# Performance work log

Hardware: AMD Instinct MI355X
Metric: run time of the kernel (lower is better)

## Reference

```python
import jax, jax.numpy as jnp
import numpy as np

D = 1024
H = 16
DH = D // H


def setup_inputs() -> dict:
    key = jax.random.key(0)
    ks = jax.random.split(key, 9)
    s = 1.0 / np.sqrt(D)
    return {
        "x": jax.random.normal(ks[0], (4, 2048, D), dtype=jnp.float32),
        "wq": jax.random.uniform(ks[1], (D, D), jnp.float32, -s, s),
        "bq": jax.random.uniform(ks[2], (D,), jnp.float32, -s, s),
        "wk": jax.random.uniform(ks[3], (D, D), jnp.float32, -s, s),
        "bk": jax.random.uniform(ks[4], (D,), jnp.float32, -s, s),
        "wv": jax.random.uniform(ks[5], (D, D), jnp.float32, -s, s),
        "bv": jax.random.uniform(ks[6], (D,), jnp.float32, -s, s),
        "wo": jax.random.uniform(ks[7], (D, D), jnp.float32, -s, s),
        "bo": jax.random.uniform(ks[8], (D,), jnp.float32, -s, s),
    }


def reference(x, wq, bq, wk, bk, wv, bv, wo, bo):
    B, S, _ = x.shape
    # projections + split heads: [B, S, D] -> [B, H, S, Dh]
    def split(t):
        return t.reshape(B, S, H, DH).transpose(0, 2, 1, 3)
    q = split(x @ wq + bq)
    k = split(x @ wk + bk)
    v = split(x @ wv + bv)
    scale = 1.0 / jnp.sqrt(jnp.float32(DH))
    scores = jnp.einsum("bhqd,bhkd->bhqk", q, k) * scale  # [B,H,S,S]
    att = jax.nn.softmax(scores, axis=-1)
    out = jnp.einsum("bhqk,bhkd->bhqd", att, v)  # [B,H,S,Dh]
    out = out.transpose(0, 2, 1, 3).reshape(B, S, D)
    return out @ wo + bo
```

## Files before the change

### kernel.cpp

```cpp
#include <hip/hip_runtime.h>
#include <stdint.h>

typedef float f32x4 __attribute__((ext_vector_type(4)));
typedef __bf16 bf16x8 __attribute__((ext_vector_type(8)));
typedef unsigned short ushort_t;
typedef ushort_t ushortx8 __attribute__((ext_vector_type(8)));
typedef ushort_t ushortx4 __attribute__((ext_vector_type(4)));

#define DEV static __device__ __forceinline__

DEV ushort_t f2bf(float f) {
  union { float f; uint32_t u; } v; v.f = f;
  uint32_t u = v.u;
  return (ushort_t)((u + 0x7FFFu + ((u >> 16) & 1u)) >> 16);
}

DEV uint32_t pkbf(float a, float b) {
  __bf16 x = (__bf16)a, y = (__bf16)b;
  return (uint32_t)__builtin_bit_cast(unsigned short, x) |
         ((uint32_t)__builtin_bit_cast(unsigned short, y) << 16);
}

DEV void cp16(const void* g, void* l) {
  __builtin_amdgcn_global_load_lds((const __attribute__((address_space(1))) unsigned int*)g,
                                   (__attribute__((address_space(3))) unsigned int*)l,
                                   16, 0, 0);
}

DEV f32x4 mfma16(bf16x8 a, bf16x8 b, f32x4 c) {
  return __builtin_amdgcn_mfma_f32_16x16x32_bf16(a, b, c, 0, 0, 0);
}

__global__ __launch_bounds__(256) void k_prep(
    const float* __restrict__ x, ushort_t* __restrict__ xb,
    const float* __restrict__ wq, const float* __restrict__ wk,
    const float* __restrict__ wv, const float* __restrict__ wo,
    ushort_t* __restrict__ wqkvT, ushort_t* __restrict__ woT) {
  __shared__ float tile[32][33];
  int b = blockIdx.x;
  if (b < 4096) {
    size_t idx = ((size_t)b * 256 + threadIdx.x) * 8;
    const float4* src = (const float4*)(x + idx);
    float4 a = src[0], c = src[1];
    ushortx8 o;
    o[0] = f2bf(a.x); o[1] = f2bf(a.y); o[2] = f2bf(a.z); o[3] = f2bf(a.w);
    o[4] = f2bf(c.x); o[5] = f2bf(c.y); o[6] = f2bf(c.z); o[7] = f2bf(c.w);
    *(ushortx8*)(xb + idx) = o;
  } else {
    int t = b - 4096;
    int which = t >> 10;
    const float* src = (which == 0) ? wq : (which == 1) ? wk : (which == 2) ? wv : wo;
    ushort_t* dst = (which == 0) ? wqkvT
                    : (which == 1) ? wqkvT + 1024 * 1024
                    : (which == 2) ? wqkvT + 2 * 1024 * 1024
                                   : woT;
    int tt = t & 1023;
    int c0 = (tt & 31) * 32, r0 = (tt >> 5) * 32;
    int tx = threadIdx.x & 31, ty = threadIdx.x >> 5;
#pragma unroll
    for (int i = ty; i < 32; i += 8)
      tile[i][tx] = src[(size_t)(r0 + i) * 1024 + c0 + tx];
    __syncthreads();
#pragma unroll
    for (int i = ty; i < 32; i += 8)
      dst[(size_t)(c0 + i) * 1024 + r0 + tx] = f2bf(tile[tx][i]);
  }
}

template <int MODE>
__global__ __launch_bounds__(512, 1) void k_gemm2(
    const ushort_t* __restrict__ A, const ushort_t* __restrict__ Bt,
    const float* __restrict__ b0, const float* __restrict__ b1,
    const float* __restrict__ b2, ushort_t* __restrict__ qw,
    ushort_t* __restrict__ kw, ushort_t* __restrict__ vtw,
    float* __restrict__ outf) {
  extern __shared__ ushort_t lds[];
  ushort_t* As3 = lds;
  ushort_t* Bs3 = lds + 3 * 8192;
  const int K = 1024, NT = 16;
  int tid = threadIdx.x;
  int w = tid >> 6, lane = tid & 63, l16 = lane & 15, lg = lane >> 4;
  int wr = w >> 2, wc = w & 3;
  int m0 = blockIdx.x * 128, n0 = blockIdx.y * 256;

  const ushort_t* Asrc = A + (size_t)(m0 + (tid >> 3)) * K +
                         (size_t)(((tid & 7) ^ ((tid >> 3) & 7)) * 8);
  const ushort_t* Bsrc = Bt + (size_t)(n0 + (tid >> 3)) * K +
                         (size_t)(((tid & 7) ^ ((tid >> 3) & 7)) * 8);

  f32x4 acc[4][4] = {};
  bf16x8 a[2][2], b[4][2];
  const int aRow = wr * 64 + l16, bRow = wc * 64 + l16, rsw = l16 & 7;

#pragma unroll
  for (int tt = 0; tt < 2; ++tt) {
    cp16(Asrc + (size_t)tt * 64, As3 + tt * 8192 + w * 512);
    cp16(Asrc + (size_t)tt * 64 + (size_t)64 * K, As3 + tt * 8192 + 4096 + w * 512);
#pragma unroll
    for (int s = 0; s < 4; ++s)
      cp16(Bsrc + (size_t)tt * 64 + (size_t)s * 64 * K,
           Bs3 + tt * 16384 + s * 4096 + w * 512);
  }
  asm volatile("s_waitcnt vmcnt(6)" ::: "memory");
  __builtin_amdgcn_s_barrier();

  int cur = 0, nx2 = 2;
  for (int t = 0; t < NT; ++t) {
    ushort_t* AsC = As3 + cur * 8192;
    ushort_t* BsC = Bs3 + cur * 16384;
    ushort_t* AsN = As3 + nx2 * 8192;
    ushort_t* BsN = Bs3 + nx2 * 16384;
    int t2 = (t + 2 < NT) ? t + 2 : NT - 1;
    const ushort_t* A2 = Asrc + (size_t)t2 * 64;
    const ushort_t* B2 = Bsrc + (size_t)t2 * 64;

#pragma unroll
    for (int i2 = 0; i2 < 2; ++i2)
#pragma unroll
      for (int ks = 0; ks < 2; ++ks)
        a[i2][ks] = *(const bf16x8*)&AsC[(aRow + i2 * 16) * 64 +
                                         (((ks << 2) | lg) ^ rsw) * 8];
#pragma unroll
    for (int j2 = 0; j2 < 2; ++j2)
#pragma unroll
      for (int ks = 0; ks < 2; ++ks)
        b[j2][ks] = *(const bf16x8*)&BsC[(bRow + j2 * 16) * 64 +
                                         (((ks << 2) | lg) ^ rsw) * 8];
    cp16(A2, AsN + w * 512);
    cp16(A2 + (size_t)64 * K, AsN + 4096 + w * 512);
    __builtin_amdgcn_s_barrier();
    asm volatile("s_waitcnt lgkmcnt(0)" ::: "memory");
    __builtin_amdgcn_s_setprio(1);
#pragma unroll
    for (int i2 = 0; i2 < 2; ++i2)
#pragma unroll
      for (int j2 = 0; j2 < 2; ++j2)
#pragma unroll
        for (int ks = 0; ks < 2; ++ks)
          acc[i2][j2] = mfma16(a[i2][ks], b[j2][ks], acc[i2][j2]);
    __builtin_amdgcn_s_setprio(0);
    __builtin_amdgcn_s_barrier();

#pragma unroll
    for (int j2 = 2; j2 < 4; ++j2)
#pragma unroll
      for (int ks = 0; ks < 2; ++ks)
        b[j2][ks] = *(const bf16x8*)&BsC[(bRow + j2 * 16) * 64 +
                                         (((ks << 2) | lg) ^ rsw) * 8];
    cp16(B2, BsN + w * 512);
    cp16(B2 + (size_t)64 * K, BsN + 4096 + w * 512);
    __builtin_amdgcn_s_barrier();
    asm volatile("s_waitcnt lgkmcnt(0)" ::: "memory");
    __builtin_amdgcn_s_setprio(1);
#pragma unroll
    for (int i2 = 0; i2 < 2; ++i2)
#pragma unroll
      for (int j2 = 2; j2 < 4; ++j2)
#pragma unroll
        for (int ks = 0; ks < 2; ++ks)
          acc[i2][j2] = mfma16(a[i2][ks], b[j2][ks], acc[i2][j2]);
    __builtin_amdgcn_s_setprio(0);
    __builtin_amdgcn_s_barrier();

#pragma unroll
    for (int i2 = 0; i2 < 2; ++i2)
#pragma unroll
      for (int ks = 0; ks < 2; ++ks)
        a[i2][ks] = *(const bf16x8*)&AsC[(aRow + (2 + i2) * 16) * 64 +
                                         (((ks << 2) | lg) ^ rsw) * 8];
    cp16(B2 + (size_t)2 * 64 * K, BsN + 8192 + w * 512);
    cp16(B2 + (size_t)3 * 64 * K, BsN + 12288 + w * 512);
    __builtin_amdgcn_s_barrier();
    asm volatile("s_waitcnt lgkmcnt(0)" ::: "memory");
    __builtin_amdgcn_s_setprio(1);
#pragma unroll
    for (int i2 = 0; i2 < 2; ++i2)
#pragma unroll
      for (int j2 = 2; j2 < 4; ++j2)
#pragma unroll
        for (int ks = 0; ks < 2; ++ks)
          acc[2 + i2][j2] = mfma16(a[i2][ks], b[j2][ks], acc[2 + i2][j2]);
    __builtin_amdgcn_s_setprio(0);
    __builtin_amdgcn_s_barrier();

    asm volatile("s_waitcnt vmcnt(6)" ::: "memory");
    __builtin_amdgcn_s_barrier();
    __builtin_amdgcn_s_setprio(1);
#pragma unroll
    for (int i2 = 0; i2 < 2; ++i2)
#pragma unroll
      for (int j2 = 0; j2 < 2; ++j2)
#pragma unroll
        for (int ks = 0; ks < 2; ++ks)
          acc[2 + i2][j2] = mfma16(a[i2][ks], b[j2][ks], acc[2 + i2][j2]);
    __builtin_amdgcn_s_setprio(0);
    __builtin_amdgcn_s_barrier();

    cur = (cur + 1 == 3) ? 0 : cur + 1;
    nx2 = (nx2 + 1 == 3) ? 0 : nx2 + 1;
  }

  if (MODE == 0) {
    const float QSCALE = 0.18033688011112042f;
    int p = blockIdx.x >> 3;
    int cbase = (m0 & 1023) + wr * 64;
    if (p == 2) {
#pragma unroll
      for (int i = 0; i < 4; ++i) {
        int oc = cbase + i * 16 + lg * 4;
        int h = oc >> 6, dh0 = oc & 63;
        float4 bb = *(const float4*)&b2[oc];
#pragma unroll
        for (int j = 0; j < 4; ++j) {
          int tok = n0 + wc * 64 + j * 16 + l16;
          int bi = tok >> 11, tk = tok & 2047;
          size_t vb = ((size_t)((bi * 16 + h) * 64 + dh0)) * 2048 + tk;
          vtw[vb] = f2bf(acc[i][j][0] + bb.x);
          vtw[vb + 2048] = f2bf(acc[i][j][1] + bb.y);
          vtw[vb + 2 * 2048] = f2bf(acc[i][j][2] + bb.z);
          vtw[vb + 3 * 2048] = f2bf(acc[i][j][3] + bb.w);
        }
      }
    } else {
      const float* bias = (p == 0) ? b0 : b1;
      ushort_t* dst = (p == 0) ? qw : kw;
      float qs = (p == 0) ? QSCALE : 1.0f;
#pragma unroll
      for (int i = 0; i < 4; ++i) {
        int oc = cbase + i * 16 + lg * 4;
        int h = oc >> 6, dh0 = oc & 63;
        float4 bb = *(const float4*)&bias[oc];
#pragma unroll
        for (int j = 0; j < 4; ++j) {
          int tok = n0 + wc * 64 + j * 16 + l16;
          size_t base =
              ((size_t)((tok >> 11) * 16 + h) * 2048 + (tok & 2047)) * 64 + dh0;
          ushortx4 pk;
          pk[0] = f2bf((acc[i][j][0] + bb.x) * qs);
          pk[1] = f2bf((acc[i][j][1] + bb.y) * qs);
          pk[2] = f2bf((acc[i][j][2] + bb.z) * qs);
          pk[3] = f2bf((acc[i][j][3] + bb.w) * qs);
          *(ushortx4*)&dst[base] = pk;
        }
      }
    }
  } else {
#pragma unroll
    for (int j = 0; j < 4; ++j) {
      int col = n0 + wc * 64 + j * 16 + l16;
      float bb = b0[col];
#pragma unroll
      for (int i = 0; i < 4; ++i) {
#pragma unroll
        for (int r = 0; r < 4; ++r) {
          int row = m0 + wr * 64 + i * 16 + lg * 4 + r;
          outf[(size_t)row * 1024 + col] = acc[i][j][r] + bb;
        }
      }
    }
  }
}

__global__ __launch_bounds__(512, 2) void k_attn(
    const ushort_t* __restrict__ qg, const ushort_t* __restrict__ kg,
    const ushort_t* __restrict__ vtg, ushort_t* __restrict__ att) {
  __shared__ ushort_t Ks[2][64 * 64];
  __shared__ ushort_t Vs[2][64 * 64];
  __shared__ ushort_t Ps[8][16 * 128];
  int tid = threadIdx.x;
  int w = tid >> 6, lane = tid & 63, l16 = lane & 15, lg = lane >> 4;
  int i = blockIdx.x;
  int bh = (i & 7) * 8 + ((i >> 3) & 7);
  int q0 = (i >> 6) * 256;
  const ushort_t* qh = qg + (size_t)bh * 2048 * 64;

  const ushort_t* kstage = kg + (size_t)bh * 2048 * 64 + (size_t)(tid >> 3) * 64 +
                           (size_t)(((tid & 7) ^ ((tid >> 3) & 7)) * 8);
  const ushort_t* vstage = vtg + (size_t)bh * 64 * 2048 + (size_t)(tid >> 3) * 2048 +
                           (size_t)(((tid & 7) ^ ((tid >> 3) & 7)) * 8);

  bf16x8 qf[2][2];
#pragma unroll
  for (int st = 0; st < 2; ++st)
#pragma unroll
    for (int ks = 0; ks < 2; ++ks)
      qf[st][ks] = *(const bf16x8*)(qh + (size_t)(q0 + w * 32 + st * 16 + l16) * 64 +
                                    ks * 32 + lg * 8);

  bf16x8 vone;
#pragma unroll
  for (int t = 0; t < 8; ++t) vone[t] = (__bf16)1.0f;

  f32x4 o[2][5] = {};

  cp16(kstage, &Ks[0][tid * 8]);
  cp16(vstage, &Vs[0][tid * 8]);
  __syncthreads();

  for (int t = 0; t < 32; ++t) {
    int cur = t & 1, nxt = cur ^ 1;
    cp16(kstage + (size_t)(t + 1) * 64 * 64, &Ks[nxt][tid * 8]);
    cp16(vstage + (size_t)(t + 1) * 64, &Vs[nxt][tid * 8]);

    f32x4 sc[2][4] = {};
    __builtin_amdgcn_s_setprio(1);
#pragma unroll
    for (int jt = 0; jt < 4; ++jt) {
      int row = jt * 16 + l16;
      bf16x8 kf0 = *(const bf16x8*)&Ks[cur][row * 64 + ((lg) ^ (l16 & 7)) * 8];
      bf16x8 kf1 = *(const bf16x8*)&Ks[cur][row * 64 + ((lg + 4) ^ (l16 & 7)) * 8];
      sc[0][jt] = mfma16(kf0, qf[0][0], sc[0][jt]);
      sc[0][jt] = mfma16(kf1, qf[0][1], sc[0][jt]);
      sc[1][jt] = mfma16(kf0, qf[1][0], sc[1][jt]);
      sc[1][jt] = mfma16(kf1, qf[1][1], sc[1][jt]);
    }
    __builtin_amdgcn_s_setprio(0);

#pragma unroll
    for (int st = 0; st < 2; ++st)
#pragma unroll
      for (int jt = 0; jt < 4; ++jt) {
        float e0 = __builtin_amdgcn_exp2f(sc[st][jt][0]);
        float e1 = __builtin_amdgcn_exp2f(sc[st][jt][1]);
        float e2 = __builtin_amdgcn_exp2f(sc[st][jt][2]);
        float e3 = __builtin_amdgcn_exp2f(sc[st][jt][3]);
        uint2 pk2;
        pk2.x = pkbf(e0, e1);
        pk2.y = pkbf(e2, e3);
        *(uint2*)&Ps[w][l16 * 128 +
                        (((st * 8 + jt * 2 + (lg >> 1)) ^ l16) * 8) +
                        (lg & 1) * 4] = pk2;
      }

    __builtin_amdgcn_s_setprio(1);
#pragma unroll
    for (int ks = 0; ks < 2; ++ks) {
      bf16x8 pf0 =
          *(const bf16x8*)&Ps[w][l16 * 128 + (((ks * 4 + lg) ^ l16) * 8)];
      bf16x8 pf1 =
          *(const bf16x8*)&Ps[w][l16 * 128 + (((8 + ks * 4 + lg) ^ l16) * 8)];
      o[0][4] = mfma16(pf0, vone, o[0][4]);
      o[1][4] = mfma16(pf1, vone, o[1][4]);
#pragma unroll
      for (int dt = 0; dt < 4; ++dt) {
        int vrow = dt * 16 + l16;
        bf16x8 vf =
            *(const bf16x8*)&Vs[cur][vrow * 64 + (((ks * 4 + lg) ^ (l16 & 7)) * 8)];
        o[0][dt] = mfma16(pf0, vf, o[0][dt]);
        o[1][dt] = mfma16(pf1, vf, o[1][dt]);
      }
    }
    __builtin_amdgcn_s_setprio(0);

    __syncthreads();
  }

  int bi = bh >> 4, h = bh & 15;
#pragma unroll
  for (int st = 0; st < 2; ++st) {
    f32x4 inv;
#pragma unroll
    for (int r = 0; r < 4; ++r) inv[r] = __builtin_amdgcn_rcpf(o[st][4][r]);
#pragma unroll
    for (int dt = 0; dt < 4; ++dt)
#pragma unroll
      for (int r = 0; r < 4; ++r) {
        int srow = q0 + w * 32 + st * 16 + lg * 4 + r;
        int col = h * 64 + dt * 16 + l16;
        att[(size_t)(bi * 2048 + srow) * 1024 + col] = f2bf(o[st][dt][r] * inv[r]);
      }
  }
}

extern "C" void kernel_launch(void* const* d_in, const int* in_sizes, int n_in,
                              void* d_out, int out_size, void* d_ws, size_t ws_size,
                              hipStream_t stream) {
  const float* x = (const float*)d_in[0];
  const float* wq = (const float*)d_in[1];
  const float* bq = (const float*)d_in[2];
  const float* wk = (const float*)d_in[3];
  const float* bk = (const float*)d_in[4];
  const float* wv = (const float*)d_in[5];
  const float* bv = (const float*)d_in[6];
  const float* wo = (const float*)d_in[7];
  const float* bo = (const float*)d_in[8];
  float* out = (float*)d_out;

  char* ws = (char*)d_ws;
  ushort_t* xb = (ushort_t*)(ws);
  ushort_t* wqkvT = (ushort_t*)(ws + 16777216);
  ushort_t* woT = (ushort_t*)(ws + 23068672);
  ushort_t* qw = (ushort_t*)(ws + 25165824);
  ushort_t* kw = (ushort_t*)(ws + 41943040);
  ushort_t* vtw = (ushort_t*)(ws + 58720256);
  ushort_t* att = (ushort_t*)(ws + 75497472);

  k_prep<<<dim3(8192), dim3(256), 0, stream>>>(x, xb, wq, wk, wv, wo, wqkvT, woT);

  const int G2_LDS = 147456;
  hipFuncSetAttribute(reinterpret_cast<const void*>(&k_gemm2<0>),
                      hipFuncAttributeMaxDynamicSharedMemorySize, G2_LDS);
  hipFuncSetAttribute(reinterpret_cast<const void*>(&k_gemm2<1>),
                      hipFuncAttributeMaxDynamicSharedMemorySize, G2_LDS);

  k_gemm2<0><<<dim3(24, 32), dim3(512), G2_LDS, stream>>>(
      wqkvT, xb, bq, bk, bv, qw, kw, vtw, nullptr);

  k_attn<<<dim3(512), dim3(512), 0, stream>>>(qw, kw, vtw, att);

  k_gemm2<1><<<dim3(64, 4), dim3(512), G2_LDS, stream>>>(
      att, woT, bo, nullptr, nullptr, nullptr, nullptr, nullptr, out);
}
```

Baseline: 259.1 us.

## Fuse prep, QKV GEMM, attention and output GEMM into one cooperative persistent kernel

Replaces four separate kernel launches with a single cooperative kernel of 256 persistent blocks that run each stage in turn, separated by grid-wide syncs. Each block loops over the QKV GEMM tiles (3 per block) and the attention units (2 per block), and does one output GEMM tile. The GEMM's clamped tail prefetches now write into a dead LDS region, and a full drain is added at the end of each tile so LDS can be reused safely. The aim is to remove launch gaps and tail effects between kernels. In exchange, attention now runs at one block per CU instead of two, and the grid syncs add cost.

```diff
diff --git a/kernel.cpp b/kernel.cpp
--- a/kernel.cpp
+++ b/kernel.cpp
@@ -1,5 +1,8 @@
 #include <hip/hip_runtime.h>
+#include <hip/hip_cooperative_groups.h>
 #include <stdint.h>
+
+namespace cg = cooperative_groups;
 
 typedef float f32x4 __attribute__((ext_vector_type(4)));
 typedef __bf16 bf16x8 __attribute__((ext_vector_type(8)));
@@ -31,57 +34,59 @@
   return __builtin_amdgcn_mfma_f32_16x16x32_bf16(a, b, c, 0, 0, 0);
 }
 
-__global__ __launch_bounds__(256) void k_prep(
-    const float* __restrict__ x, ushort_t* __restrict__ xb,
-    const float* __restrict__ wq, const float* __restrict__ wk,
-    const float* __restrict__ wv, const float* __restrict__ wo,
-    ushort_t* __restrict__ wqkvT, ushort_t* __restrict__ woT) {
-  __shared__ float tile[32][33];
-  int b = blockIdx.x;
-  if (b < 4096) {
-    size_t idx = ((size_t)b * 256 + threadIdx.x) * 8;
+#define DEAD_OFF 73728
+
+DEV void prep_phase(int bid, int tid, const float* x, ushort_t* xb,
+                    const float* wq, const float* wk, const float* wv,
+                    const float* wo, ushort_t* wqkvT, ushort_t* woT,
+                    ushort_t* lds) {
+  int gtid = bid * 512 + tid;
+  for (int c = gtid; c < 1048576; c += 131072) {
+    size_t idx = (size_t)c * 8;
     const float4* src = (const float4*)(x + idx);
-    float4 a = src[0], c = src[1];
+    float4 a = src[0], cc = src[1];
     ushortx8 o;
     o[0] = f2bf(a.x); o[1] = f2bf(a.y); o[2] = f2bf(a.z); o[3] = f2bf(a.w);
-    o[4] = f2bf(c.x); o[5] = f2bf(c.y); o[6] = f2bf(c.z); o[7] = f2bf(c.w);
+    o[4] = f2bf(cc.x); o[5] = f2bf(cc.y); o[6] = f2bf(cc.z); o[7] = f2bf(cc.w);
     *(ushortx8*)(xb + idx) = o;
-  } else {
-    int t = b - 4096;
-    int which = t >> 10;
+  }
+  float* tf = (float*)lds;
+  int sub = tid >> 8, stid = tid & 255;
+  int tx = stid & 31, ty = stid >> 5;
+  float* tile = tf + sub * 1056;
+  for (int it = 0; it < 8; ++it) {
+    int v = bid * 16 + it * 2 + sub;
+    int which = v >> 10;
     const float* src = (which == 0) ? wq : (which == 1) ? wk : (which == 2) ? wv : wo;
     ushort_t* dst = (which == 0) ? wqkvT
                     : (which == 1) ? wqkvT + 1024 * 1024
                     : (which == 2) ? wqkvT + 2 * 1024 * 1024
                                    : woT;
-    int tt = t & 1023;
+    int tt = v & 1023;
     int c0 = (tt & 31) * 32, r0 = (tt >> 5) * 32;
-    int tx = threadIdx.x & 31, ty = threadIdx.x >> 5;
+    __syncthreads();
 #pragma unroll
     for (int i = ty; i < 32; i += 8)
-      tile[i][tx] = src[(size_t)(r0 + i) * 1024 + c0 + tx];
+      tile[i * 33 + tx] = src[(size_t)(r0 + i) * 1024 + c0 + tx];
     __syncthreads();
 #pragma unroll
     for (int i = ty; i < 32; i += 8)
-      dst[(size_t)(c0 + i) * 1024 + r0 + tx] = f2bf(tile[tx][i]);
+      dst[(size_t)(c0 + i) * 1024 + r0 + tx] = f2bf(tile[tx * 33 + i]);
   }
 }
 
 template <int MODE>
-__global__ __launch_bounds__(512, 1) void k_gemm2(
-    const ushort_t* __restrict__ A, const ushort_t* __restrict__ Bt,
-    const float* __restrict__ b0, const float* __restrict__ b1,
-    const float* __restrict__ b2, ushort_t* __restrict__ qw,
-    ushort_t* __restrict__ kw, ushort_t* __restrict__ vtw,
-    float* __restrict__ outf) {
-  extern __shared__ ushort_t lds[];
+DEV void gemm_tile(const ushort_t* A, const ushort_t* Bt, const float* b0,
+                   const float* b1, const float* b2, ushort_t* qw,
+                   ushort_t* kw, ushort_t* vtw, float* outf, int bx, int by,
+                   int tid, ushort_t* lds) {
   ushort_t* As3 = lds;
   ushort_t* Bs3 = lds + 3 * 8192;
+  ushort_t* dead = lds + DEAD_OFF;
   const int K = 1024, NT = 16;
-  int tid = threadIdx.x;
   int w = tid >> 6, lane = tid & 63, l16 = lane & 15, lg = lane >> 4;
   int wr = w >> 2, wc = w & 3;
-  int m0 = blockIdx.x * 128, n0 = blockIdx.y * 256;
+  int m0 = bx * 128, n0 = by * 256;
 
   const ushort_t* Asrc = A + (size_t)(m0 + (tid >> 3)) * K +
                          (size_t)(((tid & 7) ^ ((tid >> 3) & 7)) * 8);
@@ -108,9 +113,14 @@
   for (int t = 0; t < NT; ++t) {
     ushort_t* AsC = As3 + cur * 8192;
     ushort_t* BsC = Bs3 + cur * 16384;
-    ushort_t* AsN = As3 + nx2 * 8192;
-    ushort_t* BsN = Bs3 + nx2 * 16384;
-    int t2 = (t + 2 < NT) ? t + 2 : NT - 1;
+    bool live = (t + 2 < NT);
+    ushort_t* AsN = live ? As3 + nx2 * 8192 : dead;
+    ushort_t* BsN = live ? Bs3 + nx2 * 16384 : dead;
+    int a4096 = live ? 4096 : 0;
+    int b4096 = live ? 4096 : 0;
+    int b8192 = live ? 8192 : 0;
+    int b12288 = live ? 12288 : 0;
+    int t2 = live ? t + 2 : NT - 1;
     const ushort_t* A2 = Asrc + (size_t)t2 * 64;
     const ushort_t* B2 = Bsrc + (size_t)t2 * 64;
 
@@ -127,7 +137,7 @@
         b[j2][ks] = *(const bf16x8*)&BsC[(bRow + j2 * 16) * 64 +
                                          (((ks << 2) | lg) ^ rsw) * 8];
     cp16(A2, AsN + w * 512);
-    cp16(A2 + (size_t)64 * K, AsN + 4096 + w * 512);
+    cp16(A2 + (size_t)64 * K, AsN + a4096 + w * 512);
     __builtin_amdgcn_s_barrier();
     asm volatile("s_waitcnt lgkmcnt(0)" ::: "memory");
     __builtin_amdgcn_s_setprio(1);
@@ -148,7 +158,7 @@
         b[j2][ks] = *(const bf16x8*)&BsC[(bRow + j2 * 16) * 64 +
                                          (((ks << 2) | lg) ^ rsw) * 8];
     cp16(B2, BsN + w * 512);
-    cp16(B2 + (size_t)64 * K, BsN + 4096 + w * 512);
+    cp16(B2 + (size_t)64 * K, BsN + b4096 + w * 512);
     __builtin_amdgcn_s_barrier();
     asm volatile("s_waitcnt lgkmcnt(0)" ::: "memory");
     __builtin_amdgcn_s_setprio(1);
@@ -168,8 +178,8 @@
       for (int ks = 0; ks < 2; ++ks)
         a[i2][ks] = *(const bf16x8*)&AsC[(aRow + (2 + i2) * 16) * 64 +
                                          (((ks << 2) | lg) ^ rsw) * 8];
-    cp16(B2 + (size_t)2 * 64 * K, BsN + 8192 + w * 512);
-    cp16(B2 + (size_t)3 * 64 * K, BsN + 12288 + w * 512);
+    cp16(B2 + (size_t)2 * 64 * K, BsN + b8192 + w * 512);
+    cp16(B2 + (size_t)3 * 64 * K, BsN + b12288 + w * 512);
     __builtin_amdgcn_s_barrier();
     asm volatile("s_waitcnt lgkmcnt(0)" ::: "memory");
     __builtin_amdgcn_s_setprio(1);
@@ -199,10 +209,12 @@
     cur = (cur + 1 == 3) ? 0 : cur + 1;
     nx2 = (nx2 + 1 == 3) ? 0 : nx2 + 1;
   }
+  asm volatile("s_waitcnt vmcnt(0)" ::: "memory");
+  __builtin_amdgcn_s_barrier();
 
   if (MODE == 0) {
     const float QSCALE = 0.18033688011112042f;
-    int p = blockIdx.x >> 3;
+    int p = bx >> 3;
     int cbase = (m0 & 1023) + wr * 64;
     if (p == 2) {
 #pragma unroll
@@ -261,15 +273,12 @@
   }
 }
 
-__global__ __launch_bounds__(512, 2) void k_attn(
-    const ushort_t* __restrict__ qg, const ushort_t* __restrict__ kg,
-    const ushort_t* __restrict__ vtg, ushort_t* __restrict__ att) {
-  __shared__ ushort_t Ks[2][64 * 64];
-  __shared__ ushort_t Vs[2][64 * 64];
-  __shared__ ushort_t Ps[8][16 * 128];
-  int tid = threadIdx.x;
+DEV void attn_unit(int i, const ushort_t* qg, const ushort_t* kg,
+                   const ushort_t* vtg, ushort_t* att, int tid, ushort_t* lds) {
+  ushort_t* Ks = lds;
+  ushort_t* Vs = lds + 8192;
+  ushort_t* Ps = lds + 16384;
   int w = tid >> 6, lane = tid & 63, l16 = lane & 15, lg = lane >> 4;
-  int i = blockIdx.x;
   int bh = (i & 7) * 8 + ((i >> 3) & 7);
   int q0 = (i >> 6) * 256;
   const ushort_t* qh = qg + (size_t)bh * 2048 * 64;
@@ -293,22 +302,22 @@
 
   f32x4 o[2][5] = {};
 
-  cp16(kstage, &Ks[0][tid * 8]);
-  cp16(vstage, &Vs[0][tid * 8]);
+  cp16(kstage, Ks + tid * 8);
+  cp16(vstage, Vs + tid * 8);
   __syncthreads();
 
   for (int t = 0; t < 32; ++t) {
     int cur = t & 1, nxt = cur ^ 1;
-    cp16(kstage + (size_t)(t + 1) * 64 * 64, &Ks[nxt][tid * 8]);
-    cp16(vstage + (size_t)(t + 1) * 64, &Vs[nxt][tid * 8]);
+    cp16(kstage + (size_t)(t + 1) * 64 * 64, Ks + nxt * 4096 + tid * 8);
+    cp16(vstage + (size_t)(t + 1) * 64, Vs + nxt * 4096 + tid * 8);
 
     f32x4 sc[2][4] = {};
     __builtin_amdgcn_s_setprio(1);
 #pragma unroll
     for (int jt = 0; jt < 4; ++jt) {
       int row = jt * 16 + l16;
-      bf16x8 kf0 = *(const bf16x8*)&Ks[cur][row * 64 + ((lg) ^ (l16 & 7)) * 8];
-      bf16x8 kf1 = *(const bf16x8*)&Ks[cur][row * 64 + ((lg + 4) ^ (l16 & 7)) * 8];
+      bf16x8 kf0 = *(const bf16x8*)&Ks[cur * 4096 + row * 64 + ((lg) ^ (l16 & 7)) * 8];
+      bf16x8 kf1 = *(const bf16x8*)&Ks[cur * 4096 + row * 64 + ((lg + 4) ^ (l16 & 7)) * 8];
       sc[0][jt] = mfma16(kf0, qf[0][0], sc[0][jt]);
       sc[0][jt] = mfma16(kf1, qf[0][1], sc[0][jt]);
       sc[1][jt] = mfma16(kf0, qf[1][0], sc[1][jt]);
@@ -327,25 +336,25 @@
         uint2 pk2;
         pk2.x = pkbf(e0, e1);
         pk2.y = pkbf(e2, e3);
-        *(uint2*)&Ps[w][l16 * 128 +
-                        (((st * 8 + jt * 2 + (lg >> 1)) ^ l16) * 8) +
-                        (lg & 1) * 4] = pk2;
+        *(uint2*)&Ps[w * 2048 + l16 * 128 +
+                     (((st * 8 + jt * 2 + (lg >> 1)) ^ l16) * 8) +
+                     (lg & 1) * 4] = pk2;
       }
 
     __builtin_amdgcn_s_setprio(1);
 #pragma unroll
     for (int ks = 0; ks < 2; ++ks) {
       bf16x8 pf0 =
-          *(const bf16x8*)&Ps[w][l16 * 128 + (((ks * 4 + lg) ^ l16) * 8)];
+          *(const bf16x8*)&Ps[w * 2048 + l16 * 128 + (((ks * 4 + lg) ^ l16) * 8)];
       bf16x8 pf1 =
-          *(const bf16x8*)&Ps[w][l16 * 128 + (((8 + ks * 4 + lg) ^ l16) * 8)];
+          *(const bf16x8*)&Ps[w * 2048 + l16 * 128 + (((8 + ks * 4 + lg) ^ l16) * 8)];
       o[0][4] = mfma16(pf0, vone, o[0][4]);
       o[1][4] = mfma16(pf1, vone, o[1][4]);
 #pragma unroll
       for (int dt = 0; dt < 4; ++dt) {
         int vrow = dt * 16 + l16;
-        bf16x8 vf =
-            *(const bf16x8*)&Vs[cur][vrow * 64 + (((ks * 4 + lg) ^ (l16 & 7)) * 8)];
+        bf16x8 vf = *(const bf16x8*)&Vs[cur * 4096 + vrow * 64 +
+                                        (((ks * 4 + lg) ^ (l16 & 7)) * 8)];
         o[0][dt] = mfma16(pf0, vf, o[0][dt]);
         o[1][dt] = mfma16(pf1, vf, o[1][dt]);
       }
@@ -370,6 +379,41 @@
         att[(size_t)(bi * 2048 + srow) * 1024 + col] = f2bf(o[st][dt][r] * inv[r]);
       }
   }
+}
+
+__global__ __launch_bounds__(512, 1) void k_mega(
+    const float* __restrict__ x, const float* __restrict__ wq,
+    const float* __restrict__ bq, const float* __restrict__ wk,
+    const float* __restrict__ bk, const float* __restrict__ wv,
+    const float* __restrict__ bv, const float* __restrict__ wo,
+    const float* __restrict__ bo, ushort_t* __restrict__ xb,
+    ushort_t* __restrict__ wqkvT, ushort_t* __restrict__ woT,
+    ushort_t* __restrict__ qw, ushort_t* __restrict__ kw,
+    ushort_t* __restrict__ vtw, ushort_t* __restrict__ att,
+    float* __restrict__ out) {
+  extern __shared__ ushort_t lds[];
+  cg::grid_group grid = cg::this_grid();
+  int tid = threadIdx.x, bid = blockIdx.x;
+
+  prep_phase(bid, tid, x, xb, wq, wk, wv, wo, wqkvT, woT, lds);
+  __threadfence();
+  grid.sync();
+
+  for (int rep = 0; rep < 3; ++rep) {
+    int v = bid + rep * 256;
+    gemm_tile<0>(wqkvT, xb, bq, bk, bv, qw, kw, vtw, nullptr, v % 24, v / 24,
+                 tid, lds);
+  }
+  __threadfence();
+  grid.sync();
+
+  attn_unit(bid, qw, kw, vtw, att, tid, lds);
+  attn_unit(bid + 256, qw, kw, vtw, att, tid, lds);
+  __threadfence();
+  grid.sync();
+
+  gemm_tile<1>(att, woT, bo, nullptr, nullptr, nullptr, nullptr, nullptr, out,
+               bid % 64, bid / 64, tid, lds);
 }
 
 extern "C" void kernel_launch(void* const* d_in, const int* in_sizes, int n_in,
@@ -395,19 +439,15 @@
   ushort_t* vtw = (ushort_t*)(ws + 58720256);
   ushort_t* att = (ushort_t*)(ws + 75497472);
 
-  k_prep<<<dim3(8192), dim3(256), 0, stream>>>(x, xb, wq, wk, wv, wo, wqkvT, woT);
-
-  const int G2_LDS = 147456;
-  hipFuncSetAttribute(reinterpret_cast<const void*>(&k_gemm2<0>),
-                      hipFuncAttributeMaxDynamicSharedMemorySize, G2_LDS);
-  hipFuncSetAttribute(reinterpret_cast<const void*>(&k_gemm2<1>),
-                      hipFuncAttributeMaxDynamicSharedMemorySize, G2_LDS);
-
-  k_gemm2<0><<<dim3(24, 32), dim3(512), G2_LDS, stream>>>(
-      wqkvT, xb, bq, bk, bv, qw, kw, vtw, nullptr);
-
-  k_attn<<<dim3(512), dim3(512), 0, stream>>>(qw, kw, vtw, att);
-
-  k_gemm2<1><<<dim3(64, 4), dim3(512), G2_LDS, stream>>>(
-      att, woT, bo, nullptr, nullptr, nullptr, nullptr, nullptr, out);
-}
+  const int MEGA_LDS = 155648;
+  hipFuncSetAttribute(reinterpret_cast<const void*>(&k_mega),
+                      hipFuncAttributeMaxDynamicSharedMemorySize, MEGA_LDS);
+
+  void* args[] = {(void*)&x,  (void*)&wq,    (void*)&bq,  (void*)&wk,
+                  (void*)&bk, (void*)&wv,    (void*)&bv,  (void*)&wo,
+                  (void*)&bo, (void*)&xb,    (void*)&wqkvT, (void*)&woT,
+                  (void*)&qw, (void*)&kw,    (void*)&vtw, (void*)&att,
+                  (void*)&out};
+  hipLaunchCooperativeKernel(reinterpret_cast<const void*>(&k_mega),
+                             dim3(256), dim3(512), args, MEGA_LDS, stream);
+}
```

After: 574.4 us. 2.22x slower.
